# Kernel tuning notes

Measured on AMD Instinct MI355X. Metric: run time of the kernel, lower is better.

The kernel has to match this reference:

```python
import jax, jax.numpy as jnp
import numpy as np


def setup_inputs() -> dict:
    key = jax.random.key(0)
    k1, k2, k3 = jax.random.split(key, 3)
    B, N, M = 4, 8192, 8192
    xyz1 = jax.random.normal(k1, (B, N, 3), dtype=jnp.float32)
    xyz2 = jax.random.normal(k2, (B, M, 3), dtype=jnp.float32)
    weights1 = jax.random.uniform(k3, (B, N), dtype=jnp.float32)
    return {"xyz1": xyz1, "xyz2": xyz2, "weights1": weights1}


def _min_sqdist(xyz1, xyz2):
    n2 = jnp.sum(xyz1 * xyz1, axis=-1)  # [B,N]
    m2 = jnp.sum(xyz2 * xyz2, axis=-1)  # [B,M]
    cross = jnp.einsum("bnd,bmd->bnm", xyz1, xyz2)
    sq = n2[:, :, None] + m2[:, None, :] - 2.0 * cross
    sq = jnp.maximum(sq, 0.0)  # numerical clamp, matches exact squared dist >= 0
    return jnp.min(sq, axis=2)  # [B,N] nearest-neighbor squared distance


def reference(xyz1, xyz2, weights1) -> jnp.ndarray:
    # dist1: for each point in xyz1, squared distance to nearest point in xyz2
    dist1 = jnp.sqrt(_min_sqdist(xyz1, xyz2))  # [B,N] L1 (euclidean) distances
    dist1 = dist1 * weights1
    return jnp.sum(dist1) / jnp.sum(weights1)
```

## Files before the change

kernel.cpp:

```cpp
#include <hip/hip_runtime.h>
#include <math.h>

constexpr int B = 4;
constexpr int N = 8192;
constexpr int M = 8192;
constexpr int NPTS = B * N;
constexpr int MPTS = B * M;

constexpr int TPB = 256;
constexpr int PB  = 4;
constexpr int PTS_PER_BLOCK = TPB * PB;
constexpr int NB1 = N / PTS_PER_BLOCK;
constexpr int MC  = 32;
constexpr int CHUNK = M / MC;

__global__ __launch_bounds__(TPB) void prep_kernel(
    const float* __restrict__ xyz2, float4* __restrict__ q,
    unsigned* __restrict__ minarr, float* __restrict__ acc) {
  int i = blockIdx.x * TPB + threadIdx.x;
  if (i < MPTS) {
    float x = xyz2[3 * i + 0];
    float y = xyz2[3 * i + 1];
    float z = xyz2[3 * i + 2];
    q[i] = make_float4(-2.0f * x, -2.0f * y, -2.0f * z,
                       fmaf(x, x, fmaf(y, y, z * z)));
    minarr[i] = 0x7F800000u;
  }
  if (i < 2) acc[i] = 0.0f;
}

__global__ __launch_bounds__(TPB) void chamfer_min_kernel(
    const float* __restrict__ xyz1, const float4* __restrict__ q,
    unsigned* __restrict__ minarr) {
  __shared__ float4 lq[CHUNK];

  const int t  = threadIdx.x;
  const int mc = blockIdx.x;
  const int pb = blockIdx.y;
  const int b  = blockIdx.z;

  lq[t] = q[b * M + mc * CHUNK + t];

  float x1[PB], y1[PB], z1[PB], smin[PB];
  const int base1 = b * N + pb * PTS_PER_BLOCK + t;
#pragma unroll
  for (int p = 0; p < PB; ++p) {
    int idx = base1 + p * TPB;
    x1[p] = xyz1[3 * idx + 0];
    y1[p] = xyz1[3 * idx + 1];
    z1[p] = xyz1[3 * idx + 2];
    smin[p] = INFINITY;
  }
  __syncthreads();

#pragma unroll 4
  for (int j = 0; j < CHUNK; ++j) {
    float4 v = lq[j];
#pragma unroll
    for (int p = 0; p < PB; ++p) {
      float s = fmaf(x1[p], v.x, fmaf(y1[p], v.y, fmaf(z1[p], v.z, v.w)));
      smin[p] = fminf(smin[p], s);
    }
  }

#pragma unroll
  for (int p = 0; p < PB; ++p) {
    int idx = base1 + p * TPB;
    float n2 = fmaf(x1[p], x1[p], fmaf(y1[p], y1[p], z1[p] * z1[p]));
    float d2 = fmaxf(n2 + smin[p], 0.0f);
    atomicMin(&minarr[idx], __float_as_uint(d2));
  }
}

__global__ __launch_bounds__(TPB) void reduce_kernel(
    const unsigned* __restrict__ minarr, const float* __restrict__ w,
    float* __restrict__ acc) {
  int i = blockIdx.x * TPB + threadIdx.x;
  float d  = sqrtf(__uint_as_float(minarr[i]));
  float wi = w[i];
  float num = d * wi;
  float den = wi;

#pragma unroll
  for (int off = 32; off > 0; off >>= 1) {
    num += __shfl_down(num, off, 64);
    den += __shfl_down(den, off, 64);
  }

  __shared__ float snum[TPB / 64], sden[TPB / 64];
  int wid  = threadIdx.x >> 6;
  int lane = threadIdx.x & 63;
  if (lane == 0) { snum[wid] = num; sden[wid] = den; }
  __syncthreads();
  if (threadIdx.x == 0) {
    float a = 0.0f, c = 0.0f;
#pragma unroll
    for (int k = 0; k < TPB / 64; ++k) { a += snum[k]; c += sden[k]; }
    atomicAdd(&acc[0], a);
    atomicAdd(&acc[1], c);
  }
}

__global__ void finalize_kernel(const float* __restrict__ acc,
                                float* __restrict__ out) {
  out[0] = acc[0] / acc[1];
}

extern "C" void kernel_launch(void* const* d_in, const int* in_sizes, int n_in,
                              void* d_out, int out_size, void* d_ws,
                              size_t ws_size, hipStream_t stream) {
  const float* xyz1 = (const float*)d_in[0];
  const float* xyz2 = (const float*)d_in[1];
  const float* wts  = (const float*)d_in[2];
  float* out = (float*)d_out;

  char* ws = (char*)d_ws;
  float4*   q      = (float4*)ws;
  unsigned* minarr = (unsigned*)(ws + (size_t)MPTS * sizeof(float4));
  float*    acc    = (float*)(ws + (size_t)MPTS * sizeof(float4)
                                 + (size_t)NPTS * sizeof(unsigned));

  hipLaunchKernelGGL(prep_kernel, dim3(MPTS / TPB), dim3(TPB), 0, stream,
                     xyz2, q, minarr, acc);
  hipLaunchKernelGGL(chamfer_min_kernel, dim3(MC, NB1, B), dim3(TPB), 0,
                     stream, xyz1, q, minarr);
  hipLaunchKernelGGL(reduce_kernel, dim3(NPTS / TPB), dim3(TPB), 0, stream,
                     minarr, wts, acc);
  hipLaunchKernelGGL(finalize_kernel, dim3(1), dim3(1), 0, stream, acc, out);
}
```

Measured before the change: 85.41 us.

## Use packed FMA, fuse prep into main kernel, replace atomics with partial buffers

```diff
diff --git a/kernel.cpp b/kernel.cpp
--- a/kernel.cpp
+++ b/kernel.cpp
@@ -8,75 +8,104 @@
 constexpr int MPTS = B * M;
 
 constexpr int TPB = 256;
-constexpr int PB  = 4;
+constexpr int PB  = 8;
 constexpr int PTS_PER_BLOCK = TPB * PB;
 constexpr int NB1 = N / PTS_PER_BLOCK;
-constexpr int MC  = 32;
+constexpr int MC  = 64;
 constexpr int CHUNK = M / MC;
 
-__global__ __launch_bounds__(TPB) void prep_kernel(
-    const float* __restrict__ xyz2, float4* __restrict__ q,
-    unsigned* __restrict__ minarr, float* __restrict__ acc) {
-  int i = blockIdx.x * TPB + threadIdx.x;
-  if (i < MPTS) {
-    float x = xyz2[3 * i + 0];
-    float y = xyz2[3 * i + 1];
-    float z = xyz2[3 * i + 2];
-    q[i] = make_float4(-2.0f * x, -2.0f * y, -2.0f * z,
-                       fmaf(x, x, fmaf(y, y, z * z)));
-    minarr[i] = 0x7F800000u;
-  }
-  if (i < 2) acc[i] = 0.0f;
-}
+constexpr int RB = 128;
 
-__global__ __launch_bounds__(TPB) void chamfer_min_kernel(
-    const float* __restrict__ xyz1, const float4* __restrict__ q,
-    unsigned* __restrict__ minarr) {
-  __shared__ float4 lq[CHUNK];
+typedef float v2f __attribute__((ext_vector_type(2)));
+
+__global__ __launch_bounds__(TPB, 4) void chamfer_min_kernel(
+    const float* __restrict__ xyz1, const float* __restrict__ xyz2,
+    float* __restrict__ part) {
+  __shared__ float lqx[CHUNK], lqy[CHUNK], lqz[CHUNK], lqw[CHUNK];
 
   const int t  = threadIdx.x;
   const int mc = blockIdx.x;
   const int pb = blockIdx.y;
   const int b  = blockIdx.z;
 
-  lq[t] = q[b * M + mc * CHUNK + t];
+  if (t < CHUNK) {
+    int gi = b * M + mc * CHUNK + t;
+    float x = xyz2[3 * gi + 0];
+    float y = xyz2[3 * gi + 1];
+    float z = xyz2[3 * gi + 2];
+    lqx[t] = -2.0f * x;
+    lqy[t] = -2.0f * y;
+    lqz[t] = -2.0f * z;
+    lqw[t] = fmaf(x, x, fmaf(y, y, z * z));
+  }
 
-  float x1[PB], y1[PB], z1[PB], smin[PB];
+  v2f x1b[PB], y1b[PB], z1b[PB];
+  float smin[PB];
   const int base1 = b * N + pb * PTS_PER_BLOCK + t;
 #pragma unroll
   for (int p = 0; p < PB; ++p) {
     int idx = base1 + p * TPB;
-    x1[p] = xyz1[3 * idx + 0];
-    y1[p] = xyz1[3 * idx + 1];
-    z1[p] = xyz1[3 * idx + 2];
+    float x = xyz1[3 * idx + 0];
+    float y = xyz1[3 * idx + 1];
+    float z = xyz1[3 * idx + 2];
+    x1b[p] = (v2f){x, x};
+    y1b[p] = (v2f){y, y};
+    z1b[p] = (v2f){z, z};
     smin[p] = INFINITY;
   }
   __syncthreads();
 
 #pragma unroll 4
-  for (int j = 0; j < CHUNK; ++j) {
-    float4 v = lq[j];
+  for (int j4 = 0; j4 < CHUNK / 4; ++j4) {
+    float4 vx = *(const float4*)&lqx[4 * j4];
+    float4 vy = *(const float4*)&lqy[4 * j4];
+    float4 vz = *(const float4*)&lqz[4 * j4];
+    float4 vw = *(const float4*)&lqw[4 * j4];
+
+    v2f px0 = (v2f){vx.x, vx.y}, px1 = (v2f){vx.z, vx.w};
+    v2f py0 = (v2f){vy.x, vy.y}, py1 = (v2f){vy.z, vy.w};
+    v2f pz0 = (v2f){vz.x, vz.y}, pz1 = (v2f){vz.z, vz.w};
+    v2f pw0 = (v2f){vw.x, vw.y}, pw1 = (v2f){vw.z, vw.w};
+
 #pragma unroll
     for (int p = 0; p < PB; ++p) {
-      float s = fmaf(x1[p], v.x, fmaf(y1[p], v.y, fmaf(z1[p], v.z, v.w)));
-      smin[p] = fminf(smin[p], s);
+      v2f s0 = __builtin_elementwise_fma(
+          x1b[p], px0,
+          __builtin_elementwise_fma(
+              y1b[p], py0, __builtin_elementwise_fma(z1b[p], pz0, pw0)));
+      smin[p] = fminf(fminf(s0.x, s0.y), smin[p]);
+      v2f s1 = __builtin_elementwise_fma(
+          x1b[p], px1,
+          __builtin_elementwise_fma(
+              y1b[p], py1, __builtin_elementwise_fma(z1b[p], pz1, pw1)));
+      smin[p] = fminf(fminf(s1.x, s1.y), smin[p]);
     }
   }
 
 #pragma unroll
   for (int p = 0; p < PB; ++p) {
     int idx = base1 + p * TPB;
-    float n2 = fmaf(x1[p], x1[p], fmaf(y1[p], y1[p], z1[p] * z1[p]));
+    float x = x1b[p].x, y = y1b[p].x, z = z1b[p].x;
+    float n2 = fmaf(x, x, fmaf(y, y, z * z));
     float d2 = fmaxf(n2 + smin[p], 0.0f);
-    atomicMin(&minarr[idx], __float_as_uint(d2));
+    part[(size_t)mc * NPTS + idx] = d2;
   }
 }
 
 __global__ __launch_bounds__(TPB) void reduce_kernel(
-    const unsigned* __restrict__ minarr, const float* __restrict__ w,
-    float* __restrict__ acc) {
+    const float* __restrict__ part, const float* __restrict__ w,
+    float* __restrict__ pnum, float* __restrict__ pden) {
   int i = blockIdx.x * TPB + threadIdx.x;
-  float d  = sqrtf(__uint_as_float(minarr[i]));
+
+  float m0 = INFINITY, m1 = INFINITY, m2 = INFINITY, m3 = INFINITY;
+#pragma unroll
+  for (int mc = 0; mc < MC; mc += 4) {
+    m0 = fminf(m0, part[(size_t)(mc + 0) * NPTS + i]);
+    m1 = fminf(m1, part[(size_t)(mc + 1) * NPTS + i]);
+    m2 = fminf(m2, part[(size_t)(mc + 2) * NPTS + i]);
+    m3 = fminf(m3, part[(size_t)(mc + 3) * NPTS + i]);
+  }
+  float d  = sqrtf(fminf(fminf(m0, m1), fminf(m2, m3)));
   float wi = w[i];
   float num = d * wi;
   float den = wi;
@@ -96,14 +125,26 @@
     float a = 0.0f, c = 0.0f;
 #pragma unroll
     for (int k = 0; k < TPB / 64; ++k) { a += snum[k]; c += sden[k]; }
-    atomicAdd(&acc[0], a);
-    atomicAdd(&acc[1], c);
+    pnum[blockIdx.x] = a;
+    pden[blockIdx.x] = c;
   }
 }
 
-__global__ void finalize_kernel(const float* __restrict__ acc,
-                                float* __restrict__ out) {
-  out[0] = acc[0] / acc[1];
+__global__ __launch_bounds__(RB) void finalize_kernel(
+    const float* __restrict__ pnum, const float* __restrict__ pden,
+    float* __restrict__ out) {
+  int t = threadIdx.x;
+  float num = pnum[t];
+  float den = pden[t];
+#pragma unroll
+  for (int off = 32; off > 0; off >>= 1) {
+    num += __shfl_down(num, off, 64);
+    den += __shfl_down(den, off, 64);
+  }
+  __shared__ float sn[2], sd[2];
+  if ((t & 63) == 0) { sn[t >> 6] = num; sd[t >> 6] = den; }
+  __syncthreads();
+  if (t == 0) out[0] = (sn[0] + sn[1]) / (sd[0] + sd[1]);
 }
 
 extern "C" void kernel_launch(void* const* d_in, const int* in_sizes, int n_in,
@@ -115,16 +156,14 @@
   float* out = (float*)d_out;
 
   char* ws = (char*)d_ws;
-  float4*   q      = (float4*)ws;
-  unsigned* minarr = (unsigned*)(ws + (size_t)MPTS * sizeof(float4));
-  float*    acc    = (float*)(ws + (size_t)MPTS * sizeof(float4)
-                                 + (size_t)NPTS * sizeof(unsigned));
+  float* part = (float*)ws;
+  float* pnum = (float*)(ws + (size_t)MC * NPTS * sizeof(float));
+  float* pden = pnum + RB;
 
-  hipLaunchKernelGGL(prep_kernel, dim3(MPTS / TPB), dim3(TPB), 0, stream,
-                     xyz2, q, minarr, acc);
   hipLaunchKernelGGL(chamfer_min_kernel, dim3(MC, NB1, B), dim3(TPB), 0,
-                     stream, xyz1, q, minarr);
+                     stream, xyz1, xyz2, part);
   hipLaunchKernelGGL(reduce_kernel, dim3(NPTS / TPB), dim3(TPB), 0, stream,
-                     minarr, wts, acc);
-  hipLaunchKernelGGL(finalize_kernel, dim3(1), dim3(1), 0, stream, acc, out);
+                     part, wts, pnum, pden);
+  hipLaunchKernelGGL(finalize_kernel, dim3(1), dim3(RB), 0, stream, pnum, pden,
+                     out);
 }
```

Result: slower. 90.67 us (+6.2%).
